# Optimization experiments

Measured on AMD Instinct MI355X. Metric: run time of the kernel, lower is better.

## Reference

```python
import jax, jax.numpy as jnp
import numpy as np

B, S, D, H = 2, 2048, 768, 12
DEPTH = D // H


def setup_inputs() -> dict:
    key = jax.random.key(0)
    ks = jax.random.split(key, 8)
    scale = 1.0 / np.sqrt(D)
    inp = {
        "query": jax.random.normal(ks[0], (B, S, D), jnp.float32),
        "key": jax.random.normal(ks[1], (B, S, D), jnp.float32),
        "value": jax.random.normal(ks[2], (B, S, D), jnp.float32),
        # additive mask convention: 1.0 where attention is disallowed (causal)
        "mask": jnp.triu(jnp.ones((1, 1, S, S), jnp.float32), k=1),
        "Wq": jax.random.normal(ks[3], (D, D), jnp.float32) * scale,
        "bq": jnp.zeros((D,), jnp.float32),
        "Wk": jax.random.normal(ks[4], (D, D), jnp.float32) * scale,
        "bk": jnp.zeros((D,), jnp.float32),
        "Wv": jax.random.normal(ks[5], (D, D), jnp.float32) * scale,
        "bv": jnp.zeros((D,), jnp.float32),
        "Wo": jax.random.normal(ks[6], (D, D), jnp.float32) * scale,
        "bo": jnp.zeros((D,), jnp.float32),
    }
    return inp


def _split_heads(x):
    # [B, S, D] -> [B, H, S, depth]
    b, s, _ = x.shape
    return x.reshape(b, s, H, DEPTH).transpose(0, 2, 1, 3)


def reference(query, key, value, mask, Wq, bq, Wk, bk, Wv, bv, Wo, bo):
    q = _split_heads(query @ Wq + bq)   # [B,H,S,depth]
    k = _split_heads(key @ Wk + bk)
    v = _split_heads(value @ Wv + bv)

    d_k = jnp.asarray(DEPTH, q.dtype)
    logits = jnp.einsum("bhqd,bhkd->bhqk", q, k) / jnp.sqrt(d_k)
    logits = logits + mask * -1e9
    weights = jax.nn.softmax(logits, axis=-1)          # [B,H,S,S] -- O(N^2)
    attn = jnp.einsum("bhqk,bhkd->bhqd", weights, v)    # [B,H,S,depth]

    concat = attn.transpose(0, 2, 1, 3).reshape(query.shape[0], -1, D)
    return concat @ Wo + bo
```

## Files before the change

kernel.cpp:

```cpp
#include <hip/hip_runtime.h>


typedef __bf16 bf16;
typedef __bf16 bf16x8 __attribute__((ext_vector_type(8)));
typedef __bf16 bf16x4 __attribute__((ext_vector_type(4)));
typedef float  f32x4  __attribute__((ext_vector_type(4)));

__device__ __forceinline__ void async_load16(const void* g, void* l) {
  __builtin_amdgcn_global_load_lds(
      (__attribute__((address_space(1))) void*)g,
      (__attribute__((address_space(3))) void*)l, 16, 0, 0);
}

__constant__ unsigned char chunk_tab[40] = {
  3, 4, 5, 6, 7, 8, 9, 10, 11, 12, 13, 14, 15,
  7 | 16, 8 | 16, 9 | 16, 10 | 16, 11 | 16, 12 | 16, 13 | 16, 14 | 16, 15 | 16,
  11 | 32, 12 | 32, 13 | 32, 14 | 32, 15 | 32,
  15 | 48,
  2, 6 | 16, 10 | 32, 14 | 48,
  1, 5 | 16, 9 | 32, 13 | 48,
  0, 4 | 16, 8 | 32, 12 | 48,
};

__global__ __launch_bounds__(256) void transpose_w_kernel(
    const float* __restrict__ W0, const float* __restrict__ W1,
    const float* __restrict__ W2, const float* __restrict__ W3,
    bf16* __restrict__ T0, bf16* __restrict__ T1,
    bf16* __restrict__ T2, bf16* __restrict__ T3) {
  const float* W; bf16* T;
  switch (blockIdx.z) {
    case 0: W = W0; T = T0; break;
    case 1: W = W1; T = T1; break;
    case 2: W = W2; T = T2; break;
    default: W = W3; T = T3; break;
  }
  __shared__ float tile[32][33];
  const int tx = threadIdx.x, ty = threadIdx.y;
  const int k0 = blockIdx.y * 32, n0 = blockIdx.x * 32;
#pragma unroll
  for (int j = 0; j < 32; j += 8)
    tile[ty + j][tx] = W[(size_t)(k0 + ty + j) * 768 + n0 + tx];
  __syncthreads();
#pragma unroll
  for (int j = 0; j < 32; j += 8) {
    int n = ty + j;
    T[(size_t)(n0 + n) * 768 + k0 + tx] = (bf16)tile[tx][n];
  }
}

__global__ __launch_bounds__(256) void gemm_qkv_kernel(
    const float* __restrict__ X0, const float* __restrict__ X1, const float* __restrict__ X2,
    const bf16* __restrict__ W0, const bf16* __restrict__ W1, const bf16* __restrict__ W2,
    const float* __restrict__ b0, const float* __restrict__ b1, const float* __restrict__ b2,
    bf16* __restrict__ Q, bf16* __restrict__ K, bf16* __restrict__ V) {
  __shared__ __align__(16) char smem[65536];
  const int bidx = blockIdx.x;
  const int xcd = bidx & 7, ii = bidx >> 3;
  const int nt = ii % 6, mzi = ii / 6;
  const int mz = mzi * 8 + xcd;
  const int m = mz & 31, z = mz >> 5;
  const int m0 = m * 128, n0 = nt * 128;

  const float* A   = (z == 0) ? X0 : (z == 1) ? X1 : X2;
  const bf16* Wt   = (z == 0) ? W0 : (z == 1) ? W1 : W2;
  const float* bias = (z == 0) ? b0 : (z == 1) ? b1 : b2;
  bf16* outb = (z == 0) ? Q : (z == 1) ? K : V;
  const int mode = (z == 2) ? 1 : 0;

  const int t = threadIdx.x;
  const int w = t >> 6, lane = t & 63;
  const int wm = w >> 1, wn = w & 1;
  const int quad = lane >> 4, l15 = lane & 15;
  const int srow = lane >> 3, k8p = lane & 7;

  size_t offB[4]; int ldsOffB[4];
#pragma unroll
  for (int i = 0; i < 4; ++i) {
    const int rl = w * 32 + i * 8 + srow;
    const int kk = k8p ^ (rl & 7);
    offB[i] = (size_t)(n0 + rl) * 768 + kk * 8;
    ldsOffB[i] = (w * 32 + i * 8) * 64;
  }
  const int arow0 = t >> 3;
  const int ac = t & 7;
  size_t offA[4]; int apos[4];
#pragma unroll
  for (int i = 0; i < 4; ++i) {
    const int row = arow0 + i * 32;
    offA[i] = (size_t)(m0 + row) * 768 + ac * 8;
    apos[i] = row * 64 + ((ac ^ (row & 7)) << 3);
  }

  f32x4 acc[4][4] = {};
  f32x4 pa[4], pb[4];

#pragma unroll
  for (int i = 0; i < 4; ++i) {
    pa[i] = *(const f32x4*)(A + offA[i]);
    pb[i] = *(const f32x4*)(A + offA[i] + 4);
  }
#pragma unroll
  for (int i = 0; i < 4; ++i)
    async_load16(Wt + offB[i], smem + 16384 + 2 * ldsOffB[i]);
  {
    bf16* As0 = (bf16*)smem;
#pragma unroll
    for (int i = 0; i < 4; ++i) {
      bf16x8 o;
      o[0]=(bf16)pa[i][0]; o[1]=(bf16)pa[i][1]; o[2]=(bf16)pa[i][2]; o[3]=(bf16)pa[i][3];
      o[4]=(bf16)pb[i][0]; o[5]=(bf16)pb[i][1]; o[6]=(bf16)pb[i][2]; o[7]=(bf16)pb[i][3];
      *(bf16x8*)(As0 + apos[i]) = o;
    }
  }

  for (int kidx = 0; kidx < 12; ++kidx) {
    __syncthreads();
    const int cur = (kidx & 1) * 32768;
    const int nb = ((kidx + 1) & 1) * 32768;
    if (kidx < 11) {
      const int k1 = (kidx + 1) * 64;
#pragma unroll
      for (int i = 0; i < 4; ++i) {
        pa[i] = *(const f32x4*)(A + offA[i] + k1);
        pb[i] = *(const f32x4*)(A + offA[i] + k1 + 4);
      }
#pragma unroll
      for (int i = 0; i < 4; ++i)
        async_load16(Wt + offB[i] + k1, smem + nb + 16384 + 2 * ldsOffB[i]);
    }
    const bf16* As = (const bf16*)(smem + cur);
    const bf16* Bs = (const bf16*)(smem + cur + 16384);
#pragma unroll
    for (int ks = 0; ks < 2; ++ks) {
      bf16x8 af[4], bfv[4];
      const int slot = (((ks * 4 + quad) ^ (lane & 7)) * 8);
#pragma unroll
      for (int mi = 0; mi < 4; ++mi)
        af[mi] = *(const bf16x8*)(As + (wm * 64 + mi * 16 + l15) * 64 + slot);
#pragma unroll
      for (int ni = 0; ni < 4; ++ni)
        bfv[ni] = *(const bf16x8*)(Bs + (wn * 64 + ni * 16 + l15) * 64 + slot);
#pragma unroll
      for (int mi = 0; mi < 4; ++mi)
#pragma unroll
        for (int ni = 0; ni < 4; ++ni)
          acc[mi][ni] = __builtin_amdgcn_mfma_f32_16x16x32_bf16(af[mi], bfv[ni], acc[mi][ni], 0, 0, 0);
    }
    if (kidx < 11) {
      bf16* Asn = (bf16*)(smem + nb);
#pragma unroll
      for (int i = 0; i < 4; ++i) {
        bf16x8 o;
        o[0]=(bf16)pa[i][0]; o[1]=(bf16)pa[i][1]; o[2]=(bf16)pa[i][2]; o[3]=(bf16)pa[i][3];
        o[4]=(bf16)pb[i][0]; o[5]=(bf16)pb[i][1]; o[6]=(bf16)pb[i][2]; o[7]=(bf16)pb[i][3];
        *(bf16x8*)(Asn + apos[i]) = o;
      }
    }
  }

#pragma unroll
  for (int ni = 0; ni < 4; ++ni) {
    const float bc = bias[n0 + wn * 64 + ni * 16 + l15];
#pragma unroll
    for (int mi = 0; mi < 4; ++mi)
#pragma unroll
      for (int r = 0; r < 4; ++r) acc[mi][ni][r] += bc;
  }

  __syncthreads();
  if (mode == 0) {
    bf16* Ce = (bf16*)smem;
#pragma unroll
    for (int ni = 0; ni < 4; ++ni) {
      const int col = wn * 64 + ni * 16 + l15;
#pragma unroll
      for (int mi = 0; mi < 4; ++mi) {
        const int row = wm * 64 + mi * 16 + quad * 4;
#pragma unroll
        for (int r = 0; r < 4; ++r)
          Ce[(row + r) * 136 + col] = (bf16)acc[mi][ni][r];
      }
    }
    __syncthreads();
#pragma unroll
    for (int j = 0; j < 8; ++j) {
      const int ci = j * 256 + t;
      const int row = ci >> 4, c8 = (ci & 15) * 8;
      bf16x8 vv = *(const bf16x8*)(Ce + row * 136 + c8);
      const int rg = m0 + row, cg = n0 + c8;
      const int bb = rg >> 11, s = rg & 2047;
      const int h = cg >> 6, d = cg & 63;
      *(bf16x8*)(outb + ((size_t)(bb * 12 + h) * 2048 + s) * 64 + d) = vv;
    }
  } else {
    bf16* Ct = (bf16*)smem;
#pragma unroll
    for (int ni = 0; ni < 4; ++ni) {
      const int col = wn * 64 + ni * 16 + l15;
#pragma unroll
      for (int mi = 0; mi < 4; ++mi) {
        const int row = wm * 64 + mi * 16 + quad * 4;
        bf16x4 pv;
        pv[0] = (bf16)acc[mi][ni][0]; pv[1] = (bf16)acc[mi][ni][1];
        pv[2] = (bf16)acc[mi][ni][2]; pv[3] = (bf16)acc[mi][ni][3];
        *(bf16x4*)(Ct + (size_t)col * 136 + row) = pv;
      }
    }
    __syncthreads();
#pragma unroll
    for (int j = 0; j < 8; ++j) {
      const int ci = j * 256 + t;
      const int col = ci >> 4, r8 = (ci & 15) * 8;
      bf16x8 vv = *(const bf16x8*)(Ct + col * 136 + r8);
      const int cg = n0 + col;
      const int h = cg >> 6, d = cg & 63;
      const int rg = m0 + r8;
      const int bb = rg >> 11, s = rg & 2047;
      *(bf16x8*)(outb + ((size_t)(bb * 12 + h) * 64 + d) * 2048 + s) = vv;
    }
  }
}

__global__ __launch_bounds__(256) void attn_kernel(
    const bf16* __restrict__ Qh, const bf16* __restrict__ Kh,
    const bf16* __restrict__ Vt,
    bf16* __restrict__ O0, bf16* __restrict__ O1,
    bf16* __restrict__ O2, bf16* __restrict__ O3,
    float* __restrict__ L0, float* __restrict__ L1,
    float* __restrict__ L2, float* __restrict__ L3) {
  const int ent = chunk_tab[blockIdx.x / 24];
  const int bh = blockIdx.x % 24;
  const int qt = ent & 15, c = ent >> 4;
  const int q0 = qt * 128;
  const int kt_begin = c * 8;
  const int ntiles = 2 * qt + 2;
  const int kt_end = (kt_begin + 8 < ntiles) ? kt_begin + 8 : ntiles;

  __shared__ __align__(16) char smem[49152];
  bf16* Ps = (bf16*)(smem + 32768);

  const int t = threadIdx.x;
  const int w = t >> 6, lane = t & 63, quad = lane >> 4, l15 = lane & 15;
  const int srow = lane >> 3, k8p = lane & 7;
  const bf16* Qp = Qh + (size_t)bh * (2048 * 64);
  const bf16* Kp = Kh + (size_t)bh * (2048 * 64);
  const bf16* Vp = Vt + (size_t)bh * (64 * 2048);

  size_t offK[2], offV[2];
  int ldsOff[2];
#pragma unroll
  for (int i = 0; i < 2; ++i) {
    const int rl = w * 16 + i * 8 + srow;
    const int kk = k8p ^ (rl & 7);
    offK[i] = (size_t)rl * 64 + kk * 8;
    offV[i] = (size_t)rl * 2048 + kk * 8;
    ldsOff[i] = (w * 16 + i * 8) * 64;
  }

  bf16x8 qf[2][2];
#pragma unroll
  for (int mi = 0; mi < 2; ++mi)
#pragma unroll
    for (int ks = 0; ks < 2; ++ks) {
      const int qrow = q0 + w * 32 + mi * 16 + l15;
      qf[mi][ks] = *(const bf16x8*)(Qp + (size_t)qrow * 64 + ks * 32 + quad * 8);
    }

  f32x4 o[2][4] = {};
  float lp[2] = {0.f, 0.f};
  const float sc = 0.125f * 1.44269504f;

#pragma unroll
  for (int i = 0; i < 2; ++i) {
    async_load16(Kp + offK[i] + (size_t)kt_begin * 64 * 64, smem + 2 * ldsOff[i]);
    async_load16(Vp + offV[i] + (size_t)kt_begin * 64,      smem + 8192 + 2 * ldsOff[i]);
  }

  for (int kt = kt_begin; kt < kt_end; ++kt) {
    const int k0 = kt * 64;
    const int cur = kt & 1;
    __syncthreads();
    if (kt + 1 < kt_end) {
      const int nb = cur ^ 1;
#pragma unroll
      for (int i = 0; i < 2; ++i) {
        async_load16(Kp + offK[i] + (size_t)(k0 + 64) * 64, smem + nb * 16384 + 2 * ldsOff[i]);
        async_load16(Vp + offV[i] + (k0 + 64),              smem + nb * 16384 + 8192 + 2 * ldsOff[i]);
      }
    }
    const bf16* Ks = (const bf16*)(smem + cur * 16384);
    const bf16* Vs = (const bf16*)(smem + cur * 16384 + 8192);

    f32x4 st[4][2] = {};
#pragma unroll
    for (int ks = 0; ks < 2; ++ks) {
      const int slot = (((ks * 4 + quad) ^ (lane & 7)) * 8);
      bf16x8 kf[4];
#pragma unroll
      for (int ni = 0; ni < 4; ++ni)
        kf[ni] = *(const bf16x8*)(Ks + (ni * 16 + l15) * 64 + slot);
#pragma unroll
      for (int ni = 0; ni < 4; ++ni)
#pragma unroll
        for (int mi = 0; mi < 2; ++mi)
          st[ni][mi] = __builtin_amdgcn_mfma_f32_16x16x32_bf16(kf[ni], qf[mi][ks], st[ni][mi], 0, 0, 0);
    }

    const bool diag = (k0 + 63 > q0);
#pragma unroll
    for (int mi = 0; mi < 2; ++mi) {
      const int q_local = w * 32 + mi * 16 + l15;
      const int qg = q0 + q_local;
#pragma unroll
      for (int ni = 0; ni < 4; ++ni) {
        bf16x4 pv;
#pragma unroll
        for (int r = 0; r < 4; ++r) {
          float p = __builtin_amdgcn_exp2f(st[ni][mi][r] * sc);
          if (diag && (k0 + ni * 16 + quad * 4 + r > qg)) p = 0.0f;
          lp[mi] += p;
          pv[r] = (bf16)p;
        }
        const int cc = ni * 2 + (quad >> 1);
        *(bf16x4*)(Ps + q_local * 64 + ((cc ^ (q_local & 7)) << 3) + ((quad & 1) << 2)) = pv;
      }
    }

#pragma unroll
    for (int ks = 0; ks < 2; ++ks) {
      const int slot = (((ks * 4 + quad) ^ (lane & 7)) * 8);
      bf16x8 pf[2], vfr[4];
#pragma unroll
      for (int mi = 0; mi < 2; ++mi)
        pf[mi] = *(const bf16x8*)(Ps + (w * 32 + mi * 16 + l15) * 64 + slot);
#pragma unroll
      for (int di = 0; di < 4; ++di)
        vfr[di] = *(const bf16x8*)(Vs + (di * 16 + l15) * 64 + slot);
#pragma unroll
      for (int mi = 0; mi < 2; ++mi)
#pragma unroll
        for (int di = 0; di < 4; ++di)
          o[mi][di] = __builtin_amdgcn_mfma_f32_16x16x32_bf16(pf[mi], vfr[di], o[mi][di], 0, 0, 0);
    }
  }

  bf16* Op; float* Lp_;
  switch (c) {
    case 0: Op = O0; Lp_ = L0; break;
    case 1: Op = O1; Lp_ = L1; break;
    case 2: Op = O2; Lp_ = L2; break;
    default: Op = O3; Lp_ = L3; break;
  }
  const int rows_c = 2048 - 512 * c;
  const size_t rbase = (size_t)bh * rows_c + (q0 - 512 * c);

#pragma unroll
  for (int mi = 0; mi < 2; ++mi) {
    float l = lp[mi];
    l += __shfl_xor(l, 16);
    l += __shfl_xor(l, 32);
    if (quad == 0) Lp_[rbase + w * 32 + mi * 16 + l15] = l;
#pragma unroll
    for (int di = 0; di < 4; ++di) {
      const int d = di * 16 + l15;
#pragma unroll
      for (int r = 0; r < 4; ++r) {
        const size_t row = rbase + w * 32 + mi * 16 + quad * 4 + r;
        Op[row * 64 + d] = (bf16)o[mi][di][r];
      }
    }
  }
}

__global__ __launch_bounds__(256) void lsum_kernel(
    const float* __restrict__ L0, const float* __restrict__ L1,
    const float* __restrict__ L2, const float* __restrict__ L3,
    float* __restrict__ Linv) {
  const int row = blockIdx.x * 256 + threadIdx.x;
  const int bh = row >> 11, s = row & 2047;
  float l = L0[row];
  if (s >= 512)  l += L1[(size_t)bh * 1536 + (s - 512)];
  if (s >= 1024) l += L2[(size_t)bh * 1024 + (s - 1024)];
  if (s >= 1536) l += L3[(size_t)bh * 512  + (s - 1536)];
  Linv[row] = 1.0f / l;
}

__global__ __launch_bounds__(256) void gemm_out_kernel(
    const bf16* __restrict__ O0, const bf16* __restrict__ O1,
    const bf16* __restrict__ O2, const bf16* __restrict__ O3,
    const float* __restrict__ Linv, const bf16* __restrict__ Wt,
    const float* __restrict__ bias, float* __restrict__ out) {
  __shared__ __align__(16) char smem[65536];
  const int bidx = blockIdx.x;
  const int xcd = bidx & 7, ii = bidx >> 3;
  const int nt = ii % 6, mi_ = ii / 6;
  const int m = mi_ * 8 + xcd;
  const int m0 = m * 128, n0 = nt * 128;
  const int bb = m >> 4;
  const int s0 = (m & 15) * 128;
  const int nch = 1 + (s0 >= 512) + (s0 >= 1024) + (s0 >= 1536);

  const int t = threadIdx.x;
  const int w = t >> 6, lane = t & 63;
  const int wm = w >> 1, wn = w & 1;
  const int quad = lane >> 4, l15 = lane & 15;
  const int srow = lane >> 3, k8p = lane & 7;

  size_t offB[4]; int ldsOffB[4];
#pragma unroll
  for (int i = 0; i < 4; ++i) {
    const int rl = w * 32 + i * 8 + srow;
    const int kk = k8p ^ (rl & 7);
    offB[i] = (size_t)(n0 + rl) * 768 + kk * 8;
    ldsOffB[i] = (w * 32 + i * 8) * 64;
  }
  const int arow0 = t >> 3;
  const int ac = t & 7;
  size_t ro0[4], ro1[4], ro2[4], ro3[4];
  int lrow[4], apos[4];
#pragma unroll
  for (int i = 0; i < 4; ++i) {
    const int r = arow0 + i * 32;
    const int s = s0 + r;
    ro0[i] = (size_t)s * 64 + ac * 8;
    ro1[i] = (size_t)(s - 512) * 64 + ac * 8;
    ro2[i] = (size_t)(s - 1024) * 64 + ac * 8;
    ro3[i] = (size_t)(s - 1536) * 64 + ac * 8;
    lrow[i] = s;
    apos[i] = r * 64 + ((ac ^ (r & 7)) << 3);
  }

  f32x4 acc[4][4] = {};
  bf16x8 pa0[4], pa1[4], pa2[4], pa3[4];
  float lv[4];

  auto loadA = [&](int kk) {
    const size_t bh = (size_t)(bb * 12 + kk);
#pragma unroll
    for (int i = 0; i < 4; ++i) {
      pa0[i] = *(const bf16x8*)(O0 + bh * 131072 + ro0[i]);
      lv[i] = Linv[bh * 2048 + lrow[i]];
    }
    if (nch >= 2)
#pragma unroll
      for (int i = 0; i < 4; ++i) pa1[i] = *(const bf16x8*)(O1 + bh * 98304 + ro1[i]);
    if (nch >= 3)
#pragma unroll
      for (int i = 0; i < 4; ++i) pa2[i] = *(const bf16x8*)(O2 + bh * 65536 + ro2[i]);
    if (nch >= 4)
#pragma unroll
      for (int i = 0; i < 4; ++i) pa3[i] = *(const bf16x8*)(O3 + bh * 32768 + ro3[i]);
  };
  auto writeA = [&](bf16* As) {
#pragma unroll
    for (int i = 0; i < 4; ++i) {
      float f[8];
#pragma unroll
      for (int k = 0; k < 8; ++k) f[k] = (float)pa0[i][k];
      if (nch >= 2)
#pragma unroll
        for (int k = 0; k < 8; ++k) f[k] += (float)pa1[i][k];
      if (nch >= 3)
#pragma unroll
        for (int k = 0; k < 8; ++k) f[k] += (float)pa2[i][k];
      if (nch >= 4)
#pragma unroll
        for (int k = 0; k < 8; ++k) f[k] += (float)pa3[i][k];
      bf16x8 o;
#pragma unroll
      for (int k = 0; k < 8; ++k) o[k] = (bf16)(f[k] * lv[i]);
      *(bf16x8*)(As + apos[i]) = o;
    }
  };

  loadA(0);
#pragma unroll
  for (int i = 0; i < 4; ++i)
    async_load16(Wt + offB[i], smem + 16384 + 2 * ldsOffB[i]);
  writeA((bf16*)smem);

  for (int kidx = 0; kidx < 12; ++kidx) {
    __syncthreads();
    const int cur = (kidx & 1) * 32768;
    const int nb = ((kidx + 1) & 1) * 32768;
    if (kidx < 11) {
      loadA(kidx + 1);
      const int k1 = (kidx + 1) * 64;
#pragma unroll
      for (int i = 0; i < 4; ++i)
        async_load16(Wt + offB[i] + k1, smem + nb + 16384 + 2 * ldsOffB[i]);
    }
    const bf16* As = (const bf16*)(smem + cur);
    const bf16* Bs = (const bf16*)(smem + cur + 16384);
#pragma unroll
    for (int ks = 0; ks < 2; ++ks) {
      bf16x8 af[4], bfv[4];
      const int slot = (((ks * 4 + quad) ^ (lane & 7)) * 8);
#pragma unroll
      for (int mi = 0; mi < 4; ++mi)
        af[mi] = *(const bf16x8*)(As + (wm * 64 + mi * 16 + l15) * 64 + slot);
#pragma unroll
      for (int ni = 0; ni < 4; ++ni)
        bfv[ni] = *(const bf16x8*)(Bs + (wn * 64 + ni * 16 + l15) * 64 + slot);
#pragma unroll
      for (int mi = 0; mi < 4; ++mi)
#pragma unroll
        for (int ni = 0; ni < 4; ++ni)
          acc[mi][ni] = __builtin_amdgcn_mfma_f32_16x16x32_bf16(af[mi], bfv[ni], acc[mi][ni], 0, 0, 0);
    }
    if (kidx < 11) writeA((bf16*)(smem + nb));
  }

#pragma unroll
  for (int ni = 0; ni < 4; ++ni) {
    const float bc = bias[n0 + wn * 64 + ni * 16 + l15];
#pragma unroll
    for (int mi = 0; mi < 4; ++mi)
#pragma unroll
      for (int r = 0; r < 4; ++r) acc[mi][ni][r] += bc;
  }

#pragma unroll
  for (int ni = 0; ni < 4; ++ni) {
    const int col = n0 + wn * 64 + ni * 16 + l15;
#pragma unroll
    for (int mi = 0; mi < 4; ++mi) {
      const int row = m0 + wm * 64 + mi * 16 + quad * 4;
#pragma unroll
      for (int r = 0; r < 4; ++r)
        out[(size_t)(row + r) * 768 + col] = acc[mi][ni][r];
    }
  }
}

extern "C" void kernel_launch(void* const* d_in, const int* in_sizes, int n_in,
                              void* d_out, int out_size, void* d_ws, size_t ws_size,
                              hipStream_t stream) {
  const float* query = (const float*)d_in[0];
  const float* key   = (const float*)d_in[1];
  const float* value = (const float*)d_in[2];
  const float* Wq = (const float*)d_in[4];
  const float* bq = (const float*)d_in[5];
  const float* Wk = (const float*)d_in[6];
  const float* bk = (const float*)d_in[7];
  const float* Wv = (const float*)d_in[8];
  const float* bv = (const float*)d_in[9];
  const float* Wo = (const float*)d_in[10];
  const float* bo = (const float*)d_in[11];
  float* out = (float*)d_out;

  char* ws = (char*)d_ws;
  bf16* wtq  = (bf16*)(ws);
  bf16* wtk  = (bf16*)(ws + 1179648);
  bf16* wtv  = (bf16*)(ws + 2359296);
  bf16* wto  = (bf16*)(ws + 3538944);
  bf16* Qh   = (bf16*)(ws + 4718592);
  bf16* Kh   = (bf16*)(ws + 11010048);
  bf16* Vtb  = (bf16*)(ws + 17301504);
  bf16* O0   = (bf16*)(ws + 23592960);
  bf16* O1   = (bf16*)(ws + 29884416);
  bf16* O2   = (bf16*)(ws + 34603008);
  bf16* O3   = (bf16*)(ws + 37748736);
  float* L0  = (float*)(ws + 39321600);
  float* L1  = (float*)(ws + 39518208);
  float* L2  = (float*)(ws + 39665664);
  float* L3  = (float*)(ws + 39763968);
  float* Liv = (float*)(ws + 39813120);

  transpose_w_kernel<<<dim3(24, 24, 4), dim3(32, 8), 0, stream>>>(Wq, Wk, Wv, Wo, wtq, wtk, wtv, wto);
  gemm_qkv_kernel<<<dim3(576), 256, 0, stream>>>(query, key, value, wtq, wtk, wtv, bq, bk, bv, Qh, Kh, Vtb);
  attn_kernel<<<dim3(960), 256, 0, stream>>>(Qh, Kh, Vtb, O0, O1, O2, O3, L0, L1, L2, L3);
  lsum_kernel<<<dim3(192), 256, 0, stream>>>(L0, L1, L2, L3, Liv);
  gemm_out_kernel<<<dim3(192), 256, 0, stream>>>(O0, O1, O2, O3, Liv, wto, bo, out);
}
```

Before: 204.7 us.

## Pre-convert inputs to bf16, drop double buffering, shrink LDS for occupancy

Adds a separate kernel that converts query/key/value to bf16, so the QKV GEMM can load A tiles with async global-to-LDS copies. The QKV, attention and output GEMMs drop double-buffered LDS and add launch_bounds hints for 4 blocks per CU. The epilogues are staged in halves to fit the smaller LDS. The output GEMM moves to 64-row tiles with twice as many blocks, and workspace buffers are reused across stages. This trades load/compute overlap and an extra conversion pass for higher occupancy and fewer register and LDS requirements per block.

```diff
diff --git a/kernel.cpp b/kernel.cpp
--- a/kernel.cpp
+++ b/kernel.cpp
@@ -21,6 +21,23 @@
   1, 5 | 16, 9 | 32, 13 | 48,
   0, 4 | 16, 8 | 32, 12 | 48,
 };
+
+__global__ __launch_bounds__(256) void convert_kernel(
+    const float* __restrict__ q, const float* __restrict__ k,
+    const float* __restrict__ v, bf16* __restrict__ qo,
+    bf16* __restrict__ ko, bf16* __restrict__ vo) {
+  const float* src; bf16* dst;
+  if (blockIdx.y == 0)      { src = q; dst = qo; }
+  else if (blockIdx.y == 1) { src = k; dst = ko; }
+  else                      { src = v; dst = vo; }
+  size_t i = ((size_t)blockIdx.x * 256 + threadIdx.x) * 8;
+  f32x4 a = *(const f32x4*)(src + i);
+  f32x4 b = *(const f32x4*)(src + i + 4);
+  bf16x8 o;
+  o[0]=(bf16)a[0]; o[1]=(bf16)a[1]; o[2]=(bf16)a[2]; o[3]=(bf16)a[3];
+  o[4]=(bf16)b[0]; o[5]=(bf16)b[1]; o[6]=(bf16)b[2]; o[7]=(bf16)b[3];
+  *(bf16x8*)(dst + i) = o;
+}
 
 __global__ __launch_bounds__(256) void transpose_w_kernel(
     const float* __restrict__ W0, const float* __restrict__ W1,
@@ -48,12 +65,12 @@
   }
 }
 
-__global__ __launch_bounds__(256) void gemm_qkv_kernel(
-    const float* __restrict__ X0, const float* __restrict__ X1, const float* __restrict__ X2,
+__global__ __launch_bounds__(256, 4) void gemm_qkv_kernel(
+    const bf16* __restrict__ A0, const bf16* __restrict__ A1, const bf16* __restrict__ A2,
     const bf16* __restrict__ W0, const bf16* __restrict__ W1, const bf16* __restrict__ W2,
     const float* __restrict__ b0, const float* __restrict__ b1, const float* __restrict__ b2,
     bf16* __restrict__ Q, bf16* __restrict__ K, bf16* __restrict__ V) {
-  __shared__ __align__(16) char smem[65536];
+  __shared__ __align__(16) char smem[32768];
   const int bidx = blockIdx.x;
   const int xcd = bidx & 7, ii = bidx >> 3;
   const int nt = ii % 6, mzi = ii / 6;
@@ -61,7 +78,7 @@
   const int m = mz & 31, z = mz >> 5;
   const int m0 = m * 128, n0 = nt * 128;
 
-  const float* A   = (z == 0) ? X0 : (z == 1) ? X1 : X2;
+  const bf16* A    = (z == 0) ? A0 : (z == 1) ? A1 : A2;
   const bf16* Wt   = (z == 0) ? W0 : (z == 1) ? W1 : W2;
   const float* bias = (z == 0) ? b0 : (z == 1) ? b1 : b2;
   bf16* outb = (z == 0) ? Q : (z == 1) ? K : V;
@@ -73,63 +90,29 @@
   const int quad = lane >> 4, l15 = lane & 15;
   const int srow = lane >> 3, k8p = lane & 7;
 
-  size_t offB[4]; int ldsOffB[4];
+  size_t offA[4], offB[4];
+  int ldsOff[4];
 #pragma unroll
   for (int i = 0; i < 4; ++i) {
     const int rl = w * 32 + i * 8 + srow;
     const int kk = k8p ^ (rl & 7);
+    offA[i] = (size_t)(m0 + rl) * 768 + kk * 8;
     offB[i] = (size_t)(n0 + rl) * 768 + kk * 8;
-    ldsOffB[i] = (w * 32 + i * 8) * 64;
-  }
-  const int arow0 = t >> 3;
-  const int ac = t & 7;
-  size_t offA[4]; int apos[4];
-#pragma unroll
-  for (int i = 0; i < 4; ++i) {
-    const int row = arow0 + i * 32;
-    offA[i] = (size_t)(m0 + row) * 768 + ac * 8;
-    apos[i] = row * 64 + ((ac ^ (row & 7)) << 3);
+    ldsOff[i] = (w * 32 + i * 8) * 128;
   }
 
   f32x4 acc[4][4] = {};
-  f32x4 pa[4], pb[4];
-
-#pragma unroll
-  for (int i = 0; i < 4; ++i) {
-    pa[i] = *(const f32x4*)(A + offA[i]);
-    pb[i] = *(const f32x4*)(A + offA[i] + 4);
-  }
-#pragma unroll
-  for (int i = 0; i < 4; ++i)
-    async_load16(Wt + offB[i], smem + 16384 + 2 * ldsOffB[i]);
-  {
-    bf16* As0 = (bf16*)smem;
+
+  for (int kidx = 0; kidx < 12; ++kidx) {
+    const int k1 = kidx * 64;
 #pragma unroll
     for (int i = 0; i < 4; ++i) {
-      bf16x8 o;
-      o[0]=(bf16)pa[i][0]; o[1]=(bf16)pa[i][1]; o[2]=(bf16)pa[i][2]; o[3]=(bf16)pa[i][3];
-      o[4]=(bf16)pb[i][0]; o[5]=(bf16)pb[i][1]; o[6]=(bf16)pb[i][2]; o[7]=(bf16)pb[i][3];
-      *(bf16x8*)(As0 + apos[i]) = o;
-    }
-  }
-
-  for (int kidx = 0; kidx < 12; ++kidx) {
+      async_load16(A  + offA[i] + k1, smem + ldsOff[i]);
+      async_load16(Wt + offB[i] + k1, smem + 16384 + ldsOff[i]);
+    }
     __syncthreads();
-    const int cur = (kidx & 1) * 32768;
-    const int nb = ((kidx + 1) & 1) * 32768;
-    if (kidx < 11) {
-      const int k1 = (kidx + 1) * 64;
-#pragma unroll
-      for (int i = 0; i < 4; ++i) {
-        pa[i] = *(const f32x4*)(A + offA[i] + k1);
-        pb[i] = *(const f32x4*)(A + offA[i] + k1 + 4);
-      }
-#pragma unroll
-      for (int i = 0; i < 4; ++i)
-        async_load16(Wt + offB[i] + k1, smem + nb + 16384 + 2 * ldsOffB[i]);
-    }
-    const bf16* As = (const bf16*)(smem + cur);
-    const bf16* Bs = (const bf16*)(smem + cur + 16384);
+    const bf16* As = (const bf16*)smem;
+    const bf16* Bs = (const bf16*)(smem + 16384);
 #pragma unroll
     for (int ks = 0; ks < 2; ++ks) {
       bf16x8 af[4], bfv[4];
@@ -146,16 +129,7 @@
         for (int ni = 0; ni < 4; ++ni)
           acc[mi][ni] = __builtin_amdgcn_mfma_f32_16x16x32_bf16(af[mi], bfv[ni], acc[mi][ni], 0, 0, 0);
     }
-    if (kidx < 11) {
-      bf16* Asn = (bf16*)(smem + nb);
-#pragma unroll
-      for (int i = 0; i < 4; ++i) {
-        bf16x8 o;
-        o[0]=(bf16)pa[i][0]; o[1]=(bf16)pa[i][1]; o[2]=(bf16)pa[i][2]; o[3]=(bf16)pa[i][3];
-        o[4]=(bf16)pb[i][0]; o[5]=(bf16)pb[i][1]; o[6]=(bf16)pb[i][2]; o[7]=(bf16)pb[i][3];
-        *(bf16x8*)(Asn + apos[i]) = o;
-      }
-    }
+    __syncthreads();
   }
 
 #pragma unroll
@@ -167,61 +141,72 @@
       for (int r = 0; r < 4; ++r) acc[mi][ni][r] += bc;
   }
 
-  __syncthreads();
   if (mode == 0) {
     bf16* Ce = (bf16*)smem;
 #pragma unroll
-    for (int ni = 0; ni < 4; ++ni) {
-      const int col = wn * 64 + ni * 16 + l15;
-#pragma unroll
-      for (int mi = 0; mi < 4; ++mi) {
-        const int row = wm * 64 + mi * 16 + quad * 4;
-#pragma unroll
-        for (int r = 0; r < 4; ++r)
-          Ce[(row + r) * 136 + col] = (bf16)acc[mi][ni][r];
+    for (int hh = 0; hh < 2; ++hh) {
+      if (wm == hh) {
+#pragma unroll
+        for (int ni = 0; ni < 4; ++ni) {
+          const int col = wn * 64 + ni * 16 + l15;
+#pragma unroll
+          for (int mi = 0; mi < 4; ++mi) {
+            const int row = mi * 16 + quad * 4;
+#pragma unroll
+            for (int r = 0; r < 4; ++r)
+              Ce[(row + r) * 136 + col] = (bf16)acc[mi][ni][r];
+          }
+        }
       }
-    }
-    __syncthreads();
-#pragma unroll
-    for (int j = 0; j < 8; ++j) {
-      const int ci = j * 256 + t;
-      const int row = ci >> 4, c8 = (ci & 15) * 8;
-      bf16x8 vv = *(const bf16x8*)(Ce + row * 136 + c8);
-      const int rg = m0 + row, cg = n0 + c8;
-      const int bb = rg >> 11, s = rg & 2047;
-      const int h = cg >> 6, d = cg & 63;
-      *(bf16x8*)(outb + ((size_t)(bb * 12 + h) * 2048 + s) * 64 + d) = vv;
+      __syncthreads();
+#pragma unroll
+      for (int j = 0; j < 4; ++j) {
+        const int ci = j * 256 + t;
+        const int row = ci >> 4, c8 = (ci & 15) * 8;
+        bf16x8 vv = *(const bf16x8*)(Ce + row * 136 + c8);
+        const int rg = m0 + hh * 64 + row, cg = n0 + c8;
+        const int bb = rg >> 11, s = rg & 2047;
+        const int h = cg >> 6, d = cg & 63;
+        *(bf16x8*)(outb + ((size_t)(bb * 12 + h) * 2048 + s) * 64 + d) = vv;
+      }
+      __syncthreads();
     }
   } else {
     bf16* Ct = (bf16*)smem;
 #pragma unroll
-    for (int ni = 0; ni < 4; ++ni) {
-      const int col = wn * 64 + ni * 16 + l15;
-#pragma unroll
-      for (int mi = 0; mi < 4; ++mi) {
-        const int row = wm * 64 + mi * 16 + quad * 4;
-        bf16x4 pv;
-        pv[0] = (bf16)acc[mi][ni][0]; pv[1] = (bf16)acc[mi][ni][1];
-        pv[2] = (bf16)acc[mi][ni][2]; pv[3] = (bf16)acc[mi][ni][3];
-        *(bf16x4*)(Ct + (size_t)col * 136 + row) = pv;
+    for (int hh = 0; hh < 2; ++hh) {
+      if (wm == hh) {
+#pragma unroll
+        for (int ni = 0; ni < 4; ++ni) {
+          const int col = wn * 64 + ni * 16 + l15;
+#pragma unroll
+          for (int mi = 0; mi < 4; ++mi) {
+            const int row = mi * 16 + quad * 4;
+            bf16x4 pv;
+            pv[0] = (bf16)acc[mi][ni][0]; pv[1] = (bf16)acc[mi][ni][1];
+            pv[2] = (bf16)acc[mi][ni][2]; pv[3] = (bf16)acc[mi][ni][3];
+            *(bf16x4*)(Ct + (size_t)col * 72 + row) = pv;
+          }
+        }
       }
-    }
-    __syncthreads();
-#pragma unroll
-    for (int j = 0; j < 8; ++j) {
-      const int ci = j * 256 + t;
-      const int col = ci >> 4, r8 = (ci & 15) * 8;
-      bf16x8 vv = *(const bf16x8*)(Ct + col * 136 + r8);
-      const int cg = n0 + col;
-      const int h = cg >> 6, d = cg & 63;
-      const int rg = m0 + r8;
-      const int bb = rg >> 11, s = rg & 2047;
-      *(bf16x8*)(outb + ((size_t)(bb * 12 + h) * 64 + d) * 2048 + s) = vv;
-    }
-  }
-}
-
-__global__ __launch_bounds__(256) void attn_kernel(
+      __syncthreads();
+#pragma unroll
+      for (int j = 0; j < 4; ++j) {
+        const int ci = j * 256 + t;
+        const int col = ci >> 3, r8 = (ci & 7) * 8;
+        bf16x8 vv = *(const bf16x8*)(Ct + col * 72 + r8);
+        const int cg = n0 + col;
+        const int h = cg >> 6, d = cg & 63;
+        const int rg = m0 + hh * 64 + r8;
+        const int bb = rg >> 11, s = rg & 2047;
+        *(bf16x8*)(outb + ((size_t)(bb * 12 + h) * 64 + d) * 2048 + s) = vv;
+      }
+      __syncthreads();
+    }
+  }
+}
+
+__global__ __launch_bounds__(256, 4) void attn_kernel(
     const bf16* __restrict__ Qh, const bf16* __restrict__ Kh,
     const bf16* __restrict__ Vt,
     bf16* __restrict__ O0, bf16* __restrict__ O1,
@@ -236,8 +221,8 @@
   const int ntiles = 2 * qt + 2;
   const int kt_end = (kt_begin + 8 < ntiles) ? kt_begin + 8 : ntiles;
 
-  __shared__ __align__(16) char smem[49152];
-  bf16* Ps = (bf16*)(smem + 32768);
+  __shared__ __align__(16) char smem[32768];
+  bf16* Ps = (bf16*)(smem + 16384);
 
   const int t = threadIdx.x;
   const int w = t >> 6, lane = t & 63, quad = lane >> 4, l15 = lane & 15;
@@ -254,7 +239,7 @@
     const int kk = k8p ^ (rl & 7);
     offK[i] = (size_t)rl * 64 + kk * 8;
     offV[i] = (size_t)rl * 2048 + kk * 8;
-    ldsOff[i] = (w * 16 + i * 8) * 64;
+    ldsOff[i] = (w * 16 + i * 8) * 128;
   }
 
   bf16x8 qf[2][2];
@@ -270,26 +255,16 @@
   float lp[2] = {0.f, 0.f};
   const float sc = 0.125f * 1.44269504f;
 
-#pragma unroll
-  for (int i = 0; i < 2; ++i) {
-    async_load16(Kp + offK[i] + (size_t)kt_begin * 64 * 64, smem + 2 * ldsOff[i]);
-    async_load16(Vp + offV[i] + (size_t)kt_begin * 64,      smem + 8192 + 2 * ldsOff[i]);
-  }
-
   for (int kt = kt_begin; kt < kt_end; ++kt) {
     const int k0 = kt * 64;
-    const int cur = kt & 1;
+#pragma unroll
+    for (int i = 0; i < 2; ++i) {
+      async_load16(Kp + offK[i] + (size_t)k0 * 64, smem + ldsOff[i]);
+      async_load16(Vp + offV[i] + k0,              smem + 8192 + ldsOff[i]);
+    }
     __syncthreads();
-    if (kt + 1 < kt_end) {
-      const int nb = cur ^ 1;
-#pragma unroll
-      for (int i = 0; i < 2; ++i) {
-        async_load16(Kp + offK[i] + (size_t)(k0 + 64) * 64, smem + nb * 16384 + 2 * ldsOff[i]);
-        async_load16(Vp + offV[i] + (k0 + 64),              smem + nb * 16384 + 8192 + 2 * ldsOff[i]);
-      }
-    }
-    const bf16* Ks = (const bf16*)(smem + cur * 16384);
-    const bf16* Vs = (const bf16*)(smem + cur * 16384 + 8192);
+    const bf16* Ks = (const bf16*)smem;
+    const bf16* Vs = (const bf16*)(smem + 8192);
 
     f32x4 st[4][2] = {};
 #pragma unroll
@@ -342,6 +317,7 @@
         for (int di = 0; di < 4; ++di)
           o[mi][di] = __builtin_amdgcn_mfma_f32_16x16x32_bf16(pf[mi], vfr[di], o[mi][di], 0, 0, 0);
     }
+    __syncthreads();
   }
 
   bf16* Op; float* Lp_;
@@ -385,19 +361,19 @@
   Linv[row] = 1.0f / l;
 }
 
-__global__ __launch_bounds__(256) void gemm_out_kernel(
+__global__ __launch_bounds__(256, 4) void gemm_out_kernel(
     const bf16* __restrict__ O0, const bf16* __restrict__ O1,
     const bf16* __restrict__ O2, const bf16* __restrict__ O3,
     const float* __restrict__ Linv, const bf16* __restrict__ Wt,
     const float* __restrict__ bias, float* __restrict__ out) {
-  __shared__ __align__(16) char smem[65536];
+  __shared__ __align__(16) char smem[24576];
   const int bidx = blockIdx.x;
   const int xcd = bidx & 7, ii = bidx >> 3;
-  const int nt = ii % 6, mi_ = ii / 6;
-  const int m = mi_ * 8 + xcd;
-  const int m0 = m * 128, n0 = nt * 128;
-  const int bb = m >> 4;
-  const int s0 = (m & 15) * 128;
+  const int nt = ii % 6, mg = ii / 6;
+  const int mt = mg * 8 + xcd;
+  const int m0 = mt * 64, n0 = nt * 128;
+  const int bb = mt >> 5;
+  const int s0 = (mt & 31) * 64;
   const int nch = 1 + (s0 >= 512) + (s0 >= 1024) + (s0 >= 1536);
 
   const int t = threadIdx.x;
@@ -412,110 +388,100 @@
     const int rl = w * 32 + i * 8 + srow;
     const int kk = k8p ^ (rl & 7);
     offB[i] = (size_t)(n0 + rl) * 768 + kk * 8;
-    ldsOffB[i] = (w * 32 + i * 8) * 64;
-  }
-  const int arow0 = t >> 3;
-  const int ac = t & 7;
-  size_t ro0[4], ro1[4], ro2[4], ro3[4];
-  int lrow[4], apos[4];
-#pragma unroll
-  for (int i = 0; i < 4; ++i) {
-    const int r = arow0 + i * 32;
-    const int s = s0 + r;
-    ro0[i] = (size_t)s * 64 + ac * 8;
-    ro1[i] = (size_t)(s - 512) * 64 + ac * 8;
-    ro2[i] = (size_t)(s - 1024) * 64 + ac * 8;
-    ro3[i] = (size_t)(s - 1536) * 64 + ac * 8;
-    lrow[i] = s;
-    apos[i] = r * 64 + ((ac ^ (r & 7)) << 3);
-  }
-
-  f32x4 acc[4][4] = {};
-  bf16x8 pa0[4], pa1[4], pa2[4], pa3[4];
-  float lv[4];
+    ldsOffB[i] = (w * 32 + i * 8) * 128;
+  }
+  const int arow = t >> 2;
+  const int ac2 = (t & 3) * 2;
+  const int sA = s0 + arow;
+  size_t ro0[2], ro1[2], ro2[2], ro3[2];
+  int apos[2];
+#pragma unroll
+  for (int j = 0; j < 2; ++j) {
+    const int cch = ac2 + j;
+    ro0[j] = (size_t)sA * 64 + cch * 8;
+    ro1[j] = (size_t)(sA - 512) * 64 + cch * 8;
+    ro2[j] = (size_t)(sA - 1024) * 64 + cch * 8;
+    ro3[j] = (size_t)(sA - 1536) * 64 + cch * 8;
+    apos[j] = arow * 64 + ((cch ^ (arow & 7)) << 3);
+  }
+
+  f32x4 acc[2][4] = {};
+  bf16x8 pa0[2], pa1[2], pa2[2], pa3[2];
+  float lv;
 
   auto loadA = [&](int kk) {
     const size_t bh = (size_t)(bb * 12 + kk);
-#pragma unroll
-    for (int i = 0; i < 4; ++i) {
-      pa0[i] = *(const bf16x8*)(O0 + bh * 131072 + ro0[i]);
-      lv[i] = Linv[bh * 2048 + lrow[i]];
-    }
+    lv = Linv[bh * 2048 + sA];
+#pragma unroll
+    for (int j = 0; j < 2; ++j) pa0[j] = *(const bf16x8*)(O0 + bh * 131072 + ro0[j]);
     if (nch >= 2)
 #pragma unroll
-      for (int i = 0; i < 4; ++i) pa1[i] = *(const bf16x8*)(O1 + bh * 98304 + ro1[i]);
+      for (int j = 0; j < 2; ++j) pa1[j] = *(const bf16x8*)(O1 + bh * 98304 + ro1[j]);
     if (nch >= 3)
 #pragma unroll
-      for (int i = 0; i < 4; ++i) pa2[i] = *(const bf16x8*)(O2 + bh * 65536 + ro2[i]);
+      for (int j = 0; j < 2; ++j) pa2[j] = *(const bf16x8*)(O2 + bh * 65536 + ro2[j]);
     if (nch >= 4)
 #pragma unroll
-      for (int i = 0; i < 4; ++i) pa3[i] = *(const bf16x8*)(O3 + bh * 32768 + ro3[i]);
+      for (int j = 0; j < 2; ++j) pa3[j] = *(const bf16x8*)(O3 + bh * 32768 + ro3[j]);
   };
-  auto writeA = [&](bf16* As) {
-#pragma unroll
-    for (int i = 0; i < 4; ++i) {
+  auto writeA = [&]() {
+    bf16* As = (bf16*)smem;
+#pragma unroll
+    for (int j = 0; j < 2; ++j) {
       float f[8];
 #pragma unroll
-      for (int k = 0; k < 8; ++k) f[k] = (float)pa0[i][k];
+      for (int k = 0; k < 8; ++k) f[k] = (float)pa0[j][k];
       if (nch >= 2)
 #pragma unroll
-        for (int k = 0; k < 8; ++k) f[k] += (float)pa1[i][k];
+        for (int k = 0; k < 8; ++k) f[k] += (float)pa1[j][k];
       if (nch >= 3)
 #pragma unroll
-        for (int k = 0; k < 8; ++k) f[k] += (float)pa2[i][k];
+        for (int k = 0; k < 8; ++k) f[k] += (float)pa2[j][k];
       if (nch >= 4)
 #pragma unroll
-        for (int k = 0; k < 8; ++k) f[k] += (float)pa3[i][k];
+        for (int k = 0; k < 8; ++k) f[k] += (float)pa3[j][k];
       bf16x8 o;
 #pragma unroll
-      for (int k = 0; k < 8; ++k) o[k] = (bf16)(f[k] * lv[i]);
-      *(bf16x8*)(As + apos[i]) = o;
+      for (int k = 0; k < 8; ++k) o[k] = (bf16)(f[k] * lv);
+      *(bf16x8*)(As + apos[j]) = o;
     }
   };
 
   loadA(0);
-#pragma unroll
-  for (int i = 0; i < 4; ++i)
-    async_load16(Wt + offB[i], smem + 16384 + 2 * ldsOffB[i]);
-  writeA((bf16*)smem);
-
   for (int kidx = 0; kidx < 12; ++kidx) {
+    writeA();
+    const int k1 = kidx * 64;
+#pragma unroll
+    for (int i = 0; i < 4; ++i)
+      async_load16(Wt + offB[i] + k1, smem + 8192 + ldsOffB[i]);
     __syncthreads();
-    const int cur = (kidx & 1) * 32768;
-    const int nb = ((kidx + 1) & 1) * 32768;
-    if (kidx < 11) {
-      loadA(kidx + 1);
-      const int k1 = (kidx + 1) * 64;
-#pragma unroll
-      for (int i = 0; i < 4; ++i)
-        async_load16(Wt + offB[i] + k1, smem + nb + 16384 + 2 * ldsOffB[i]);
-    }
-    const bf16* As = (const bf16*)(smem + cur);
-    const bf16* Bs = (const bf16*)(smem + cur + 16384);
+    if (kidx < 11) loadA(kidx + 1);
+    const bf16* As = (const bf16*)smem;
+    const bf16* Bs = (const bf16*)(smem + 8192);
 #pragma unroll
     for (int ks = 0; ks < 2; ++ks) {
-      bf16x8 af[4], bfv[4];
+      bf16x8 af[2], bfv[4];
       const int slot = (((ks * 4 + quad) ^ (lane & 7)) * 8);
 #pragma unroll
-      for (int mi = 0; mi < 4; ++mi)
-        af[mi] = *(const bf16x8*)(As + (wm * 64 + mi * 16 + l15) * 64 + slot);
+      for (int mi = 0; mi < 2; ++mi)
+        af[mi] = *(const bf16x8*)(As + (wm * 32 + mi * 16 + l15) * 64 + slot);
 #pragma unroll
       for (int ni = 0; ni < 4; ++ni)
         bfv[ni] = *(const bf16x8*)(Bs + (wn * 64 + ni * 16 + l15) * 64 + slot);
 #pragma unroll
-      for (int mi = 0; mi < 4; ++mi)
+      for (int mi = 0; mi < 2; ++mi)
 #pragma unroll
         for (int ni = 0; ni < 4; ++ni)
           acc[mi][ni] = __builtin_amdgcn_mfma_f32_16x16x32_bf16(af[mi], bfv[ni], acc[mi][ni], 0, 0, 0);
     }
-    if (kidx < 11) writeA((bf16*)(smem + nb));
+    __syncthreads();
   }
 
 #pragma unroll
   for (int ni = 0; ni < 4; ++ni) {
     const float bc = bias[n0 + wn * 64 + ni * 16 + l15];
 #pragma unroll
-    for (int mi = 0; mi < 4; ++mi)
+    for (int mi = 0; mi < 2; ++mi)
 #pragma unroll
       for (int r = 0; r < 4; ++r) acc[mi][ni][r] += bc;
   }
@@ -524,8 +490,8 @@
   for (int ni = 0; ni < 4; ++ni) {
     const int col = n0 + wn * 64 + ni * 16 + l15;
 #pragma unroll
-    for (int mi = 0; mi < 4; ++mi) {
-      const int row = m0 + wm * 64 + mi * 16 + quad * 4;
+    for (int mi = 0; mi < 2; ++mi) {
+      const int row = m0 + wm * 32 + mi * 16 + quad * 4;
 #pragma unroll
       for (int r = 0; r < 4; ++r)
         out[(size_t)(row + r) * 768 + col] = acc[mi][ni][r];
@@ -550,26 +516,30 @@
   float* out = (float*)d_out;
 
   char* ws = (char*)d_ws;
-  bf16* wtq  = (bf16*)(ws);
-  bf16* wtk  = (bf16*)(ws + 1179648);
-  bf16* wtv  = (bf16*)(ws + 2359296);
-  bf16* wto  = (bf16*)(ws + 3538944);
-  bf16* Qh   = (bf16*)(ws + 4718592);
-  bf16* Kh   = (bf16*)(ws + 11010048);
-  bf16* Vtb  = (bf16*)(ws + 17301504);
-  bf16* O0   = (bf16*)(ws + 23592960);
-  bf16* O1   = (bf16*)(ws + 29884416);
-  bf16* O2   = (bf16*)(ws + 34603008);
-  bf16* O3   = (bf16*)(ws + 37748736);
-  float* L0  = (float*)(ws + 39321600);
-  float* L1  = (float*)(ws + 39518208);
-  float* L2  = (float*)(ws + 39665664);
-  float* L3  = (float*)(ws + 39763968);
-  float* Liv = (float*)(ws + 39813120);
-
+  bf16* qb   = (bf16*)(ws);
+  bf16* kb   = (bf16*)(ws + 6291456);
+  bf16* vb   = (bf16*)(ws + 12582912);
+  bf16* O0   = (bf16*)(ws);
+  bf16* O1   = (bf16*)(ws + 6291456);
+  bf16* O2   = (bf16*)(ws + 11010048);
+  bf16* O3   = (bf16*)(ws + 14155776);
+  float* L0  = (float*)(ws + 15728640);
+  float* L1  = (float*)(ws + 15925248);
+  float* L2  = (float*)(ws + 16072704);
+  float* L3  = (float*)(ws + 16171008);
+  float* Liv = (float*)(ws + 16220160);
+  bf16* wtq  = (bf16*)(ws + 18874368);
+  bf16* wtk  = (bf16*)(ws + 20054016);
+  bf16* wtv  = (bf16*)(ws + 21233664);
+  bf16* wto  = (bf16*)(ws + 22413312);
+  bf16* Qh   = (bf16*)(ws + 23592960);
+  bf16* Kh   = (bf16*)(ws + 29884416);
+  bf16* Vtb  = (bf16*)(ws + 36175872);
+
+  convert_kernel<<<dim3(1536, 3), 256, 0, stream>>>(query, key, value, qb, kb, vb);
   transpose_w_kernel<<<dim3(24, 24, 4), dim3(32, 8), 0, stream>>>(Wq, Wk, Wv, Wo, wtq, wtk, wtv, wto);
-  gemm_qkv_kernel<<<dim3(576), 256, 0, stream>>>(query, key, value, wtq, wtk, wtv, bq, bk, bv, Qh, Kh, Vtb);
+  gemm_qkv_kernel<<<dim3(576), 256, 0, stream>>>(qb, kb, vb, wtq, wtk, wtv, bq, bk, bv, Qh, Kh, Vtb);
   attn_kernel<<<dim3(960), 256, 0, stream>>>(Qh, Kh, Vtb, O0, O1, O2, O3, L0, L1, L2, L3);
   lsum_kernel<<<dim3(192), 256, 0, stream>>>(L0, L1, L2, L3, Liv);
-  gemm_out_kernel<<<dim3(192), 256, 0, stream>>>(O0, O1, O2, O3, Liv, wto, bo, out);
-}
+  gemm_out_kernel<<<dim3(384), 256, 0, stream>>>(O0, O1, O2, O3, Liv, wto, bo, out);
+}
```

New measurement: 189.2 us. 1.08x faster.
